# Kernel tuning notes

Measured on AMD Instinct MI355X. Metric: run time of the kernel, lower is better.

The kernel has to match this reference:

```python
import jax, jax.numpy as jnp
import numpy as np

B, H, W = 1, 352, 1216
T = 6          # prop_time
CG = 8         # guidance channels per step
K = 9          # 3x3 propagation kernel


def _conv(x, w, b, pad, groups=1):
    out = jax.lax.conv_general_dilated(
        x, w, (1, 1), [(pad, pad), (pad, pad)],
        dimension_numbers=('NCHW', 'OIHW', 'NCHW'),
        feature_group_count=groups)
    return out if b is None else out + b[None, :, None, None]


def setup_inputs() -> dict:
    key = jax.random.key(0)
    ks = iter(jax.random.split(key, 32))
    def r(shape, s=0.1):
        return jax.random.normal(next(ks), shape, jnp.float32) * s
    return dict(
        feat_init=r((B, 1, H, W), 1.0),
        guidance=r((B, T * CG, H, W), 1.0),
        attn=r((B, 16, H, W), 1.0),
        feat_fix=r((B, 1, H, W), 1.0),
        aff_w_w=r((T, K, CG, 3, 3)), aff_w_b=r((T, K)),
        aff_o_w=r((T, 2 * (K - 1), CG, 3, 3)), aff_o_b=r((T, 2 * (K - 1))),
        proj_w=r((6, 3, 1, 1)),
        bn_gamma=jnp.ones((6,), jnp.float32), bn_beta=jnp.zeros((6,), jnp.float32),
        bn_mean=jnp.zeros((6,), jnp.float32), bn_var=jnp.ones((6,), jnp.float32),
        lsk0_w=r((22, 1, 1, 1)), lsk0_b=r((22,)),
        lsks_w=r((22, 1, 3, 3)), lsks_b=r((22,)),
        lsk1_w=r((11, 22, 1, 1)), lsk1_b=r((11,)),
        lsk2_w=r((11, 22, 1, 1)), lsk2_b=r((11,)),
        lsksq_w=r((2, 2, 3, 3)), lsksq_b=r((2,)),
        lskc_w=r((3, 11, 1, 1)), lskc_b=r((3,)),
    )


def _forward(feat_init, guidance, attn,
             aff_w_w, aff_w_b, aff_o_w, aff_o_b,
             proj_w, bn_gamma, bn_beta, bn_mean, bn_var,
             lsk0_w, lsk0_b, lsks_w, lsks_b, lsk1_w, lsk1_b,
             lsk2_w, lsk2_b, lsksq_w, lsksq_b, lskc_w, lskc_b):
    Bs, _, Hs, Ws = feat_init.shape
    # split guidance into T chunks of CG channels -> (T,B,CG,H,W)
    g = guidance.reshape(Bs, T, CG, Hs, Ws).transpose(1, 0, 2, 3, 4)

    def aff_fn(g_t, ww, wb, ow, ob):
        w = jax.nn.sigmoid(_conv(g_t, ww, wb, 1))              # (B,9,H,W)
        w = w / (w.sum(1, keepdims=True) + 1e-8)
        o = _conv(g_t, ow, ob, 1).reshape(Bs, K - 1, 2, Hs, Ws)
        zero = jnp.zeros((Bs, 1, 2, Hs, Ws), o.dtype)          # reference pixel
        o = jnp.concatenate([o[:, :4], zero, o[:, 4:]], 1).reshape(Bs, 2 * K, Hs, Ws)
        return o, w

    offs, affs = jax.vmap(aff_fn)(g, aff_w_w, aff_w_b, aff_o_w, aff_o_b)

    # modulated deformable conv, weight = ones(1,1,3,3), bias = 0, stride=1, pad=1
    ky = (jnp.repeat(jnp.arange(3), 3) - 1).astype(feat_init.dtype)  # (9,)
    kx = (jnp.tile(jnp.arange(3), 3) - 1).astype(feat_init.dtype)
    yy = jnp.arange(Hs, dtype=feat_init.dtype)
    xx = jnp.arange(Ws, dtype=feat_init.dtype)
    bidx = jnp.arange(Bs)[:, None, None, None]

    def dcn(feat, off, aff):
        img = feat[:, 0]                                       # (B,H,W)
        ys = yy[None, None, :, None] + ky[None, :, None, None] + off[:, 0::2]
        xs = xx[None, None, None, :] + kx[None, :, None, None] + off[:, 1::2]
        y0 = jnp.floor(ys); x0 = jnp.floor(xs)
        wy = ys - y0; wx = xs - x0
        y0i = y0.astype(jnp.int32); x0i = x0.astype(jnp.int32)
        def g4(yi, xi):
            valid = (yi >= 0) & (yi < Hs) & (xi >= 0) & (xi < Ws)
            v = img[bidx, jnp.clip(yi, 0, Hs - 1), jnp.clip(xi, 0, Ws - 1)]
            return v * valid.astype(v.dtype)
        samp = (g4(y0i, x0i) * (1 - wy) * (1 - wx)
                + g4(y0i, x0i + 1) * (1 - wy) * wx
                + g4(y0i + 1, x0i) * wy * (1 - wx)
                + g4(y0i + 1, x0i + 1) * wy * wx)
        return (aff * samp).sum(1)[:, None]                    # (B,1,H,W)

    def step(f, ox):
        o, a = ox
        fn = dcn(f, o, a)
        return fn, fn

    _, feats = jax.lax.scan(step, feat_init.astype(jnp.float32), (offs, affs))

    # combine(list_feat[3:6], attn)
    x3 = jnp.concatenate([feats[3], feats[4], feats[5]], 1)    # (B,3,H,W)
    sf = _conv(x3, proj_w, None, 0)                            # conv 3->6, no bias
    sf = (sf - bn_mean[None, :, None, None]) * jax.lax.rsqrt(bn_var + 1e-5)[None, :, None, None] \
         * bn_gamma[None, :, None, None] + bn_beta[None, :, None, None]
    sf = jnp.where(sf >= 0, sf, 0.2 * sf)                      # LeakyReLU(0.2)
    x22 = jnp.concatenate([attn, sf], 1)                       # (B,22,H,W)

    a1 = _conv(x22, lsk0_w, lsk0_b, 0, 22)                     # depthwise 1x1
    a2 = _conv(a1, lsks_w, lsks_b, 1, 22)                      # depthwise 3x3
    a1 = _conv(a1, lsk1_w, lsk1_b, 0)                          # 22->11
    a2 = _conv(a2, lsk2_w, lsk2_b, 0)                          # 22->11
    cat = jnp.concatenate([a1, a2], 1)
    agg = jnp.concatenate([cat.mean(1, keepdims=True), cat.max(1, keepdims=True)], 1)
    sig = jax.nn.sigmoid(_conv(agg, lsksq_w, lsksq_b, 1))
    at = a1 * sig[:, 0:1] + a2 * sig[:, 1:2]
    at = _conv(at, lskc_w, lskc_b, 0)                          # 11->3
    return (x3 * at).sum(1, keepdims=True)                     # (B,1,H,W)


def reference(feat_init, guidance, attn, feat_fix,
              aff_w_w, aff_w_b, aff_o_w, aff_o_b,
              proj_w, bn_gamma, bn_beta, bn_mean, bn_var,
              lsk0_w, lsk0_b, lsks_w, lsks_b, lsk1_w, lsk1_b,
              lsk2_w, lsk2_b, lsksq_w, lsksq_b, lskc_w, lskc_b):
    # feat_fix only feeds an unused mask path (if False branch) in the original
    return _forward(feat_init, guidance, attn,
                    aff_w_w, aff_w_b, aff_o_w, aff_o_b,
                    proj_w, bn_gamma, bn_beta, bn_mean, bn_var,
                    lsk0_w, lsk0_b, lsks_w, lsks_b, lsk1_w, lsk1_b,
                    lsk2_w, lsk2_b, lsksq_w, lsksq_b, lskc_w, lskc_b)
```

## Files before the change

### kernel.cpp

```cpp
#include <hip/hip_runtime.h>
#include <hip/hip_bf16.h>

#define HH 352
#define WW 1216
#define HWSZ (HH * WW)
#define TT 6

#define WS_CW   16
#define WS_TW   11008
#define WS_FB   12032

typedef __attribute__((ext_vector_type(4))) float f32x4;
typedef __attribute__((ext_vector_type(8))) short s16x8;
union FU { unsigned int u[4]; s16x8 v; };

__device__ inline float ld_in(const void* p, long long i, int bf) {
    return bf ? __bfloat162float(((const __hip_bfloat16*)p)[i]) : ((const float*)p)[i];
}

__device__ inline unsigned int bfsplit_pack(float v) {
    unsigned int uv = __float_as_uint(v);
    unsigned int h = (uv + 0x7FFFu + ((uv >> 16) & 1u)) >> 16;
    float hf = __uint_as_float(h << 16);
    float r = v - hf;
    unsigned int ur = __float_as_uint(r);
    unsigned int l = (ur + 0x7FFFu + ((ur >> 16) & 1u)) >> 16;
    return (h & 0xFFFFu) | (l << 16);
}

__device__ inline int detect_mode(const void* guid) {
    const unsigned int* u = (const unsigned int*)guid;
    int cnt = 0;
    for (int i = 0; i < 128; ++i) {
        unsigned int lo = u[i] & 0xFFFFu;
        int e = (int)((lo >> 7) & 0xFF);
        if (e >= 110 && e <= 140) cnt++;
    }
    return (cnt >= 96) ? 1 : 0;
}

__global__ void prep_small(const void* guid,
                           const void* aww, const void* awb, const void* aow, const void* aob,
                           const void* projw, const void* bng, const void* bnb,
                           const void* bnm, const void* bnv,
                           const void* l0w, const void* l0b, const void* lsw, const void* lsb,
                           const void* l1w, const void* l1b, const void* l2w, const void* l2b,
                           const void* sqw, const void* sqb, const void* lcw, const void* lcb,
                           float* ws) {
    __shared__ int smode;
    if (threadIdx.x == 0) {
        int mode = detect_mode(guid);
        smode = mode;
        if (blockIdx.x == 0) *(int*)ws = mode;
    }
    __syncthreads();
    const int bf = smode;
    const int tid = blockIdx.x * blockDim.x + threadIdx.x;
    const int stp = gridDim.x * blockDim.x;
    float* cw = ws + WS_CW;
    for (int idx = tid; idx < TT * 9 * 72; idx += stp) {
        int t = idx / 648; int r = idx % 648;
        int co = r / 72; int ci = (r % 72) / 9; int tap = r % 9;
        cw[t * 1825 + 25 + co * 72 + ci * 9 + tap] = ld_in(aww, idx, bf);
    }
    for (int idx = tid; idx < TT * 16 * 72; idx += stp) {
        int t = idx / 1152; int r = idx % 1152;
        int co = r / 72; int ci = (r % 72) / 9; int tap = r % 9;
        cw[t * 1825 + 25 + (9 + co) * 72 + ci * 9 + tap] = ld_in(aow, idx, bf);
    }
    for (int idx = tid; idx < TT * 9; idx += stp)
        cw[(idx / 9) * 1825 + (idx % 9)] = ld_in(awb, idx, bf);
    for (int idx = tid; idx < TT * 16; idx += stp)
        cw[(idx / 16) * 1825 + 9 + (idx % 16)] = ld_in(aob, idx, bf);

    float* tw = ws + WS_TW;
    for (int i = tid; i < 18; i += stp) tw[i] = ld_in(projw, i, bf);
    for (int i = tid; i < 6; i += stp) {
        float sc = ld_in(bng, i, bf) * rsqrtf(ld_in(bnv, i, bf) + 1e-5f);
        tw[18 + i] = sc;
        tw[24 + i] = ld_in(bnb, i, bf) - ld_in(bnm, i, bf) * sc;
    }
    for (int i = tid; i < 22;  i += stp) tw[32  + i] = ld_in(l0w, i, bf);
    for (int i = tid; i < 22;  i += stp) tw[54  + i] = ld_in(l0b, i, bf);
    for (int i = tid; i < 198; i += stp) tw[76  + i] = ld_in(lsw, i, bf);
    for (int i = tid; i < 22;  i += stp) tw[274 + i] = ld_in(lsb, i, bf);
    for (int i = tid; i < 242; i += stp) tw[296 + i] = ld_in(l1w, i, bf);
    for (int i = tid; i < 11;  i += stp) tw[538 + i] = ld_in(l1b, i, bf);
    for (int i = tid; i < 242; i += stp) tw[549 + i] = ld_in(l2w, i, bf);
    for (int i = tid; i < 11;  i += stp) tw[791 + i] = ld_in(l2b, i, bf);
    for (int i = tid; i < 36;  i += stp) tw[802 + i] = ld_in(sqw, i, bf);
    for (int i = tid; i < 2;   i += stp) tw[838 + i] = ld_in(sqb, i, bf);
    for (int i = tid; i < 33;  i += stp) tw[840 + i] = ld_in(lcw, i, bf);
    for (int i = tid; i < 3;   i += stp) tw[873 + i] = ld_in(lcb, i, bf);
}

__global__ void prep_feat(const void* __restrict__ feat_init, const int* __restrict__ flagp,
                          float* __restrict__ dst) {
    int bf = *flagp;
    int i = blockIdx.x * 256 + threadIdx.x;
    if (i < HWSZ) dst[i] = ld_in(feat_init, i, bf);
}

__device__ inline float samp(const float* __restrict__ src, int y, int x) {
    bool valid = (y >= 0) & (y < HH) & (x >= 0) & (x < WW);
    int yc = min(max(y, 0), HH - 1);
    int xc = min(max(x, 0), WW - 1);
    float v = src[yc * WW + xc];
    return valid ? v : 0.0f;
}

__global__ __launch_bounds__(256) void dcn_fused(
        const void* __restrict__ guid, const int* __restrict__ flagp,
        const float* __restrict__ wts,
        const float* __restrict__ src, float* __restrict__ dst, int t) {
    __shared__ unsigned int hal[8][10][36];
    __shared__ float outb[4][64][27];
    const int bf = *flagp;
    const int bx = blockIdx.x % 38, by = blockIdx.x / 38;
    const int x0 = bx * 32, y0 = by * 8;
    for (int idx = threadIdx.x; idx < 8 * 360; idx += 256) {
        int ci = idx / 360; int r = (idx % 360) / 36; int c = idx % 36;
        int gy = y0 - 1 + r, gx = x0 - 1 + c;
        float v = 0.f;
        if (c < 34 && gy >= 0 && gy < HH && gx >= 0 && gx < WW)
            v = ld_in(guid, (long long)(t * 8 + ci) * HWSZ + gy * WW + gx, bf);
        hal[ci][r][c] = bfsplit_pack(v);
    }
    const int lane = threadIdx.x & 63;
    const int wave = threadIdx.x >> 6;
    const int col = lane & 15, g = lane >> 4;

    FU Bh[2][3], Bl[2][3];
#pragma unroll
    for (int Nt = 0; Nt < 2; ++Nt)
#pragma unroll
    for (int c = 0; c < 3; ++c) {
        unsigned short eh[8], el[8];
#pragma unroll
        for (int j = 0; j < 8; ++j) {
            int ci = 2 * g + (j >> 2), dx = j & 3;
            int cc = Nt * 16 + col;
            float w = 0.f;
            if (cc < 25 && dx < 3) w = wts[25 + cc * 72 + ci * 9 + c * 3 + dx];
            unsigned int pk = bfsplit_pack(w);
            eh[j] = (unsigned short)(pk & 0xFFFFu);
            el[j] = (unsigned short)(pk >> 16);
        }
#pragma unroll
        for (int q = 0; q < 4; ++q) {
            Bh[Nt][c].u[q] = (unsigned int)eh[2*q] | ((unsigned int)eh[2*q+1] << 16);
            Bl[Nt][c].u[q] = (unsigned int)el[2*q] | ((unsigned int)el[2*q+1] << 16);
        }
    }
    __syncthreads();

    const float* bias = wts;
#pragma unroll
    for (int m = 0; m < 4; ++m) {
        const int M = wave * 4 + m;
        const int py = M >> 1;
        const int pxx = (M & 1) * 16 + col;
        FU Ah[3], Al[3];
#pragma unroll
        for (int c = 0; c < 3; ++c) {
            const unsigned int* r0 = &hal[2 * g][py + c][pxx];
            const unsigned int* r1 = &hal[2 * g + 1][py + c][pxx];
            unsigned int q0 = r0[0], q1 = r0[1], q2 = r0[2], q3 = r0[3];
            unsigned int q4 = r1[0], q5 = r1[1], q6 = r1[2], q7 = r1[3];
            Ah[c].u[0] = __builtin_amdgcn_perm(q1, q0, 0x05040100u);
            Ah[c].u[1] = __builtin_amdgcn_perm(q3, q2, 0x05040100u);
            Ah[c].u[2] = __builtin_amdgcn_perm(q5, q4, 0x05040100u);
            Ah[c].u[3] = __builtin_amdgcn_perm(q7, q6, 0x05040100u);
            Al[c].u[0] = __builtin_amdgcn_perm(q1, q0, 0x07060302u);
            Al[c].u[1] = __builtin_amdgcn_perm(q3, q2, 0x07060302u);
            Al[c].u[2] = __builtin_amdgcn_perm(q5, q4, 0x07060302u);
            Al[c].u[3] = __builtin_amdgcn_perm(q7, q6, 0x07060302u);
        }
#pragma unroll
        for (int Nt = 0; Nt < 2; ++Nt) {
            f32x4 acc = {0.f, 0.f, 0.f, 0.f};
#pragma unroll
            for (int c = 0; c < 3; ++c) {
                acc = __builtin_amdgcn_mfma_f32_16x16x32_bf16(Ah[c].v, Bh[Nt][c].v, acc, 0, 0, 0);
                acc = __builtin_amdgcn_mfma_f32_16x16x32_bf16(Al[c].v, Bh[Nt][c].v, acc, 0, 0, 0);
                acc = __builtin_amdgcn_mfma_f32_16x16x32_bf16(Ah[c].v, Bl[Nt][c].v, acc, 0, 0, 0);
            }
            const int co = Nt * 16 + col;
            if (co < 25) {
                float bs = bias[co];
#pragma unroll
                for (int r = 0; r < 4; ++r)
                    outb[wave][m * 16 + g * 4 + r][co] = acc[r] + bs;
            }
        }
    }
    __syncthreads();
    {
        const int pl = lane;
        const int Ml = pl >> 4, rd = pl & 15;
        const int M = wave * 4 + Ml;
        const int py = M >> 1;
        const int pxx = (M & 1) * 16 + rd;
        const int gy = y0 + py, gx = x0 + pxx;
        float v[25];
#pragma unroll
        for (int c = 0; c < 25; ++c) v[c] = outb[wave][pl][c];
        float w9[9], s = 0.f;
#pragma unroll
        for (int k = 0; k < 9; ++k) { w9[k] = 1.f / (1.f + __expf(-v[k])); s += w9[k]; }
        const float inv = 1.f / (s + 1e-8f);
        float out = 0.f;
#pragma unroll
        for (int k = 0; k < 9; ++k) {
            float oy = 0.f, ox = 0.f;
            if (k != 4) {
                int kp = (k < 4) ? k : (k - 1);
                oy = v[9 + 2 * kp];
                ox = v[10 + 2 * kp];
            }
            float ys = (float)(gy + k / 3 - 1) + oy;
            float xs = (float)(gx + k % 3 - 1) + ox;
            float yf = floorf(ys), xf = floorf(xs);
            float wy = ys - yf, wx = xs - xf;
            int yi = (int)yf, xi = (int)xf;
            float v00 = samp(src, yi, xi);
            float v01 = samp(src, yi, xi + 1);
            float v10 = samp(src, yi + 1, xi);
            float v11 = samp(src, yi + 1, xi + 1);
            float sv = v00 * (1.f - wy) * (1.f - wx) + v01 * (1.f - wy) * wx
                     + v10 * wy * (1.f - wx) + v11 * wy * wx;
            out = fmaf(w9[k] * inv, sv, out);
        }
        dst[gy * WW + gx] = out;
    }
}

__global__ __launch_bounds__(256) void tail1(
        const void* __restrict__ attn, const int* __restrict__ flagp,
        const float* __restrict__ tw, const float* __restrict__ feats,
        float* __restrict__ a1) {
    const int bf = *flagp;
    const int p = blockIdx.x * 256 + threadIdx.x;
    float x3[3] = { feats[3 * HWSZ + p], feats[4 * HWSZ + p], feats[5 * HWSZ + p] };
    float sf[6];
#pragma unroll
    for (int j = 0; j < 6; ++j) {
        float v = tw[j * 3 + 0] * x3[0] + tw[j * 3 + 1] * x3[1] + tw[j * 3 + 2] * x3[2];
        v = v * tw[18 + j] + tw[24 + j];
        sf[j] = (v >= 0.0f) ? v : 0.2f * v;
    }
#pragma unroll
    for (int c = 0; c < 22; ++c) {
        float x = (c < 16) ? ld_in(attn, (long long)c * HWSZ + p, bf) : sf[c - 16];
        a1[c * HWSZ + p] = fmaf(x, tw[32 + c], tw[54 + c]);
    }
}

__global__ __launch_bounds__(256) void tail2(
        const float* __restrict__ tw, const float* __restrict__ a1,
        float* __restrict__ a11, float* __restrict__ a21, float* __restrict__ agg) {
    __shared__ float tile[10][34];
    const int bx = blockIdx.x % 38, by = blockIdx.x / 38;
    const int x0 = bx * 32, y0 = by * 8;
    const int lx = threadIdx.x % 32, ly = threadIdx.x / 32;
    float acc1[11], acc2[11];
#pragma unroll
    for (int j = 0; j < 11; ++j) { acc1[j] = tw[538 + j]; acc2[j] = tw[791 + j]; }
    for (int c = 0; c < 22; ++c) {
        __syncthreads();
        for (int idx = threadIdx.x; idx < 340; idx += 256) {
            int r = idx / 34, cc = idx % 34;
            int gy = y0 - 1 + r, gx = x0 - 1 + cc;
            tile[r][cc] = (gy >= 0 && gy < HH && gx >= 0 && gx < WW)
                          ? a1[c * HWSZ + gy * WW + gx] : 0.0f;
        }
        __syncthreads();
        float a1c = tile[ly + 1][lx + 1];
        float a2c = tw[274 + c];
#pragma unroll
        for (int dy = 0; dy < 3; ++dy)
#pragma unroll
            for (int dx = 0; dx < 3; ++dx)
                a2c = fmaf(tile[ly + dy][lx + dx], tw[76 + c * 9 + dy * 3 + dx], a2c);
#pragma unroll
        for (int j = 0; j < 11; ++j) {
            acc1[j] = fmaf(a1c, tw[296 + j * 22 + c], acc1[j]);
            acc2[j] = fmaf(a2c, tw[549 + j * 22 + c], acc2[j]);
        }
    }
    const int p = (y0 + ly) * WW + x0 + lx;
    float s = 0.0f, mx = -1e30f;
#pragma unroll
    for (int j = 0; j < 11; ++j) {
        a11[j * HWSZ + p] = acc1[j];
        a21[j * HWSZ + p] = acc2[j];
        s += acc1[j] + acc2[j];
        mx = fmaxf(mx, fmaxf(acc1[j], acc2[j]));
    }
    agg[p] = s * (1.0f / 22.0f);
    agg[HWSZ + p] = mx;
}

__global__ __launch_bounds__(256) void tail3(
        const int* __restrict__ flagp, const float* __restrict__ tw,
        const float* __restrict__ feats,
        const float* __restrict__ a11, const float* __restrict__ a21,
        const float* __restrict__ agg, void* __restrict__ out) {
    __shared__ float t0[10][34], t1[10][34];
    const int bx = blockIdx.x % 38, by = blockIdx.x / 38;
    const int x0 = bx * 32, y0 = by * 8;
    for (int idx = threadIdx.x; idx < 340; idx += 256) {
        int r = idx / 34, cc = idx % 34;
        int gy = y0 - 1 + r, gx = x0 - 1 + cc;
        bool ok = (gy >= 0 && gy < HH && gx >= 0 && gx < WW);
        t0[r][cc] = ok ? agg[gy * WW + gx] : 0.0f;
        t1[r][cc] = ok ? agg[HWSZ + gy * WW + gx] : 0.0f;
    }
    __syncthreads();
    const int lx = threadIdx.x % 32, ly = threadIdx.x / 32;
    float s0 = tw[838], s1 = tw[839];
#pragma unroll
    for (int dy = 0; dy < 3; ++dy)
#pragma unroll
        for (int dx = 0; dx < 3; ++dx) {
            float v0 = t0[ly + dy][lx + dx], v1 = t1[ly + dy][lx + dx];
            s0 = fmaf(v0, tw[802 + 0 * 18 + 0 * 9 + dy * 3 + dx], s0);
            s0 = fmaf(v1, tw[802 + 0 * 18 + 1 * 9 + dy * 3 + dx], s0);
            s1 = fmaf(v0, tw[802 + 1 * 18 + 0 * 9 + dy * 3 + dx], s1);
            s1 = fmaf(v1, tw[802 + 1 * 18 + 1 * 9 + dy * 3 + dx], s1);
        }
    float sg0 = 1.0f / (1.0f + __expf(-s0));
    float sg1 = 1.0f / (1.0f + __expf(-s1));
    const int p = (y0 + ly) * WW + x0 + lx;
    float at3[3] = { tw[873], tw[874], tw[875] };
#pragma unroll
    for (int j = 0; j < 11; ++j) {
        float at = a11[j * HWSZ + p] * sg0 + a21[j * HWSZ + p] * sg1;
#pragma unroll
        for (int i = 0; i < 3; ++i) at3[i] = fmaf(at, tw[840 + i * 11 + j], at3[i]);
    }
    float o = feats[3 * HWSZ + p] * at3[0] + feats[4 * HWSZ + p] * at3[1]
            + feats[5 * HWSZ + p] * at3[2];
    int bf = *flagp;
    if (bf) ((__hip_bfloat16*)out)[p] = __float2bfloat16(o);
    else    ((float*)out)[p] = o;
}

extern "C" void kernel_launch(void* const* d_in, const int* in_sizes, int n_in,
                              void* d_out, int out_size, void* d_ws, size_t ws_size,
                              hipStream_t stream) {
    (void)in_sizes; (void)n_in; (void)out_size; (void)ws_size;
    float* WSF = (float*)d_ws;
    const int* flagp = (const int*)d_ws;
    float* cw   = WSF + WS_CW;
    float* tw   = WSF + WS_TW;
    float* FB   = WSF + WS_FB;
    float* A1   = FB + 7 * HWSZ;
    float* A11  = A1 + 22 * HWSZ;
    float* A21  = A11 + 11 * HWSZ;
    float* AGG  = A21 + 11 * HWSZ;

    prep_small<<<32, 256, 0, stream>>>(d_in[1],
        d_in[4], d_in[5], d_in[6], d_in[7],
        d_in[8], d_in[9], d_in[10], d_in[11], d_in[12],
        d_in[13], d_in[14], d_in[15], d_in[16],
        d_in[17], d_in[18], d_in[19], d_in[20],
        d_in[21], d_in[22], d_in[23], d_in[24], WSF);
    prep_feat<<<(HWSZ + 255) / 256, 256, 0, stream>>>(d_in[0], flagp, FB + 6 * HWSZ);

    for (int t = 0; t < 6; ++t) {
        const float* src = (t == 0) ? (FB + 6 * HWSZ) : (FB + (t - 1) * HWSZ);
        dcn_fused<<<44 * 38, 256, 0, stream>>>(d_in[1], flagp, cw + t * 1825, src, FB + t * HWSZ, t);
    }
    tail1<<<HWSZ / 256, 256, 0, stream>>>(d_in[2], flagp, tw, FB, A1);
    tail2<<<44 * 38, 256, 0, stream>>>(tw, A1, A11, A21, AGG);
    tail3<<<44 * 38, 256, 0, stream>>>(flagp, tw, FB, A11, A21, AGG, d_out);
}
```

Before: 484.4 us.

## Merge prep kernels, vectorize guidance halo loads, spread DCN taps across lane groups

The two prep kernels become one launch, so feat_init conversion and weight packing share a single dispatch. In fp32 mode the dcn_fused guidance halo is now loaded with float4 reads instead of scalar loads. The deformable sampling epilogue now runs per 16-pixel M tile right after its MMA, with the 9 taps split across the four 16-lane groups and reduced by shuffles. This shrinks the outb buffer and spreads gather latency over more lanes, at the cost of redundant lanes, extra shuffles and a larger grid for the merged prep kernel.

```diff
diff --git a/kernel.cpp b/kernel.cpp
--- a/kernel.cpp
+++ b/kernel.cpp
@@ -39,14 +39,15 @@
     return (cnt >= 96) ? 1 : 0;
 }
 
-__global__ void prep_small(const void* guid,
-                           const void* aww, const void* awb, const void* aow, const void* aob,
-                           const void* projw, const void* bng, const void* bnb,
-                           const void* bnm, const void* bnv,
-                           const void* l0w, const void* l0b, const void* lsw, const void* lsb,
-                           const void* l1w, const void* l1b, const void* l2w, const void* l2b,
-                           const void* sqw, const void* sqb, const void* lcw, const void* lcb,
-                           float* ws) {
+__global__ __launch_bounds__(256) void prep_all(
+        const void* feat_init, const void* guid,
+        const void* aww, const void* awb, const void* aow, const void* aob,
+        const void* projw, const void* bng, const void* bnb,
+        const void* bnm, const void* bnv,
+        const void* l0w, const void* l0b, const void* lsw, const void* lsb,
+        const void* l1w, const void* l1b, const void* l2w, const void* l2b,
+        const void* sqw, const void* sqb, const void* lcw, const void* lcb,
+        float* ws) {
     __shared__ int smode;
     if (threadIdx.x == 0) {
         int mode = detect_mode(guid);
@@ -55,8 +56,13 @@
     }
     __syncthreads();
     const int bf = smode;
-    const int tid = blockIdx.x * blockDim.x + threadIdx.x;
-    const int stp = gridDim.x * blockDim.x;
+    {
+        int i = blockIdx.x * 256 + threadIdx.x;
+        if (i < HWSZ) ws[WS_FB + 6 * HWSZ + i] = ld_in(feat_init, i, bf);
+    }
+    if (blockIdx.x >= 32) return;
+    const int tid = blockIdx.x * 256 + threadIdx.x;
+    const int stp = 32 * 256;
     float* cw = ws + WS_CW;
     for (int idx = tid; idx < TT * 9 * 72; idx += stp) {
         int t = idx / 648; int r = idx % 648;
@@ -94,13 +100,6 @@
     for (int i = tid; i < 3;   i += stp) tw[873 + i] = ld_in(lcb, i, bf);
 }
 
-__global__ void prep_feat(const void* __restrict__ feat_init, const int* __restrict__ flagp,
-                          float* __restrict__ dst) {
-    int bf = *flagp;
-    int i = blockIdx.x * 256 + threadIdx.x;
-    if (i < HWSZ) dst[i] = ld_in(feat_init, i, bf);
-}
-
 __device__ inline float samp(const float* __restrict__ src, int y, int x) {
     bool valid = (y >= 0) & (y < HH) & (x >= 0) & (x < WW);
     int yc = min(max(y, 0), HH - 1);
@@ -114,17 +113,45 @@
         const float* __restrict__ wts,
         const float* __restrict__ src, float* __restrict__ dst, int t) {
     __shared__ unsigned int hal[8][10][36];
-    __shared__ float outb[4][64][27];
+    __shared__ float outb[4][2][16][27];
     const int bf = *flagp;
     const int bx = blockIdx.x % 38, by = blockIdx.x / 38;
     const int x0 = bx * 32, y0 = by * 8;
-    for (int idx = threadIdx.x; idx < 8 * 360; idx += 256) {
-        int ci = idx / 360; int r = (idx % 360) / 36; int c = idx % 36;
-        int gy = y0 - 1 + r, gx = x0 - 1 + c;
-        float v = 0.f;
-        if (c < 34 && gy >= 0 && gy < HH && gx >= 0 && gx < WW)
-            v = ld_in(guid, (long long)(t * 8 + ci) * HWSZ + gy * WW + gx, bf);
-        hal[ci][r][c] = bfsplit_pack(v);
+
+    if (!bf) {
+        const float* gp = (const float*)guid + (long long)(t * 8) * HWSZ;
+        for (int idx = threadIdx.x; idx < 800; idx += 256) {
+            int ci = idx / 100; int rem = idx % 100; int rr = rem / 10; int k = rem % 10;
+            int gy = y0 - 1 + rr;
+            int gxb = x0 - 4 + 4 * k;
+            float vx = 0.f, vy = 0.f, vz = 0.f, vw = 0.f;
+            if (gy >= 0 && gy < HH) {
+                const float* rowp = gp + (long long)ci * HWSZ + (long long)gy * WW;
+                if (gxb >= 0 && gxb + 3 < WW) {
+                    const float4 v4 = *(const float4*)(rowp + gxb);
+                    vx = v4.x; vy = v4.y; vz = v4.z; vw = v4.w;
+                } else {
+                    if (gxb + 0 >= 0 && gxb + 0 < WW) vx = rowp[gxb + 0];
+                    if (gxb + 1 >= 0 && gxb + 1 < WW) vy = rowp[gxb + 1];
+                    if (gxb + 2 >= 0 && gxb + 2 < WW) vz = rowp[gxb + 2];
+                    if (gxb + 3 >= 0 && gxb + 3 < WW) vw = rowp[gxb + 3];
+                }
+            }
+            int c0 = 4 * k - 3;
+            if (c0 + 0 >= 0 && c0 + 0 < 36) hal[ci][rr][c0 + 0] = bfsplit_pack(vx);
+            if (c0 + 1 >= 0 && c0 + 1 < 36) hal[ci][rr][c0 + 1] = bfsplit_pack(vy);
+            if (c0 + 2 >= 0 && c0 + 2 < 36) hal[ci][rr][c0 + 2] = bfsplit_pack(vz);
+            if (c0 + 3 >= 0 && c0 + 3 < 36) hal[ci][rr][c0 + 3] = bfsplit_pack(vw);
+        }
+    } else {
+        for (int idx = threadIdx.x; idx < 8 * 360; idx += 256) {
+            int ci = idx / 360; int r = (idx % 360) / 36; int c = idx % 36;
+            int gy = y0 - 1 + r, gx = x0 - 1 + c;
+            float v = 0.f;
+            if (c < 34 && gy >= 0 && gy < HH && gx >= 0 && gx < WW)
+                v = ld_in(guid, (long long)(t * 8 + ci) * HWSZ + gy * WW + gx, bf);
+            hal[ci][r][c] = bfsplit_pack(v);
+        }
     }
     const int lane = threadIdx.x & 63;
     const int wave = threadIdx.x >> 6;
@@ -159,7 +186,8 @@
     for (int m = 0; m < 4; ++m) {
         const int M = wave * 4 + m;
         const int py = M >> 1;
-        const int pxx = (M & 1) * 16 + col;
+        const int xoff = (M & 1) * 16;
+        const int pxx = xoff + col;
         FU Ah[3], Al[3];
 #pragma unroll
         for (int c = 0; c < 3; ++c) {
@@ -190,48 +218,60 @@
                 float bs = bias[co];
 #pragma unroll
                 for (int r = 0; r < 4; ++r)
-                    outb[wave][m * 16 + g * 4 + r][co] = acc[r] + bs;
+                    outb[wave][m & 1][g * 4 + r][co] = acc[r] + bs;
             }
         }
-    }
-    __syncthreads();
-    {
-        const int pl = lane;
-        const int Ml = pl >> 4, rd = pl & 15;
-        const int M = wave * 4 + Ml;
-        const int py = M >> 1;
-        const int pxx = (M & 1) * 16 + rd;
-        const int gy = y0 + py, gx = x0 + pxx;
-        float v[25];
-#pragma unroll
-        for (int c = 0; c < 25; ++c) v[c] = outb[wave][pl][c];
-        float w9[9], s = 0.f;
-#pragma unroll
-        for (int k = 0; k < 9; ++k) { w9[k] = 1.f / (1.f + __expf(-v[k])); s += w9[k]; }
-        const float inv = 1.f / (s + 1e-8f);
-        float out = 0.f;
-#pragma unroll
-        for (int k = 0; k < 9; ++k) {
-            float oy = 0.f, ox = 0.f;
-            if (k != 4) {
-                int kp = (k < 4) ? k : (k - 1);
-                oy = v[9 + 2 * kp];
-                ox = v[10 + 2 * kp];
+        {
+            const int px = col;
+            const int gy = y0 + py;
+            const int gx = x0 + xoff + px;
+            const float* ob = &outb[wave][m & 1][px][0];
+            float sg[3], oyv[3], oxv[3];
+            float psum = 0.f;
+#pragma unroll
+            for (int i = 0; i < 3; ++i) {
+                int tap = i * 4 + g;
+                bool valid = tap < 9;
+                int tc = valid ? tap : 8;
+                float wv = ob[tc];
+                float sgv = 1.f / (1.f + __expf(-wv));
+                sg[i] = valid ? sgv : 0.f;
+                psum += sg[i];
+                int kp = (tap < 4) ? tap : tap - 1;
+                kp = min(kp, 7);
+                float oy = ob[9 + 2 * kp];
+                float ox = ob[10 + 2 * kp];
+                bool use_off = valid && (tap != 4);
+                oyv[i] = use_off ? oy : 0.f;
+                oxv[i] = use_off ? ox : 0.f;
             }
-            float ys = (float)(gy + k / 3 - 1) + oy;
-            float xs = (float)(gx + k % 3 - 1) + ox;
-            float yf = floorf(ys), xf = floorf(xs);
-            float wy = ys - yf, wx = xs - xf;
-            int yi = (int)yf, xi = (int)xf;
-            float v00 = samp(src, yi, xi);
-            float v01 = samp(src, yi, xi + 1);
-            float v10 = samp(src, yi + 1, xi);
-            float v11 = samp(src, yi + 1, xi + 1);
-            float sv = v00 * (1.f - wy) * (1.f - wx) + v01 * (1.f - wy) * wx
-                     + v10 * wy * (1.f - wx) + v11 * wy * wx;
-            out = fmaf(w9[k] * inv, sv, out);
-        }
-        dst[gy * WW + gx] = out;
+            psum += __shfl_xor(psum, 16);
+            psum += __shfl_xor(psum, 32);
+            const float inv = 1.f / (psum + 1e-8f);
+            float out = 0.f;
+#pragma unroll
+            for (int i = 0; i < 3; ++i) {
+                int tap = min(i * 4 + g, 8);
+                float w = sg[i] * inv;
+                int d3 = tap / 3;
+                int dy = d3 - 1, dx = tap - 3 * d3 - 1;
+                float ys = (float)(gy + dy) + oyv[i];
+                float xs = (float)(gx + dx) + oxv[i];
+                float yf = floorf(ys), xf = floorf(xs);
+                float wy = ys - yf, wx = xs - xf;
+                int yi = (int)yf, xi = (int)xf;
+                float v00 = samp(src, yi, xi);
+                float v01 = samp(src, yi, xi + 1);
+                float v10 = samp(src, yi + 1, xi);
+                float v11 = samp(src, yi + 1, xi + 1);
+                float sv = v00 * (1.f - wy) * (1.f - wx) + v01 * (1.f - wy) * wx
+                         + v10 * wy * (1.f - wx) + v11 * wy * wx;
+                out = fmaf(w, sv, out);
+            }
+            out += __shfl_xor(out, 16);
+            out += __shfl_xor(out, 32);
+            if (g == 0) dst[gy * WW + gx] = out;
+        }
     }
 }
 
@@ -360,13 +400,12 @@
     float* A21  = A11 + 11 * HWSZ;
     float* AGG  = A21 + 11 * HWSZ;
 
-    prep_small<<<32, 256, 0, stream>>>(d_in[1],
+    prep_all<<<1672, 256, 0, stream>>>(d_in[0], d_in[1],
         d_in[4], d_in[5], d_in[6], d_in[7],
         d_in[8], d_in[9], d_in[10], d_in[11], d_in[12],
         d_in[13], d_in[14], d_in[15], d_in[16],
         d_in[17], d_in[18], d_in[19], d_in[20],
         d_in[21], d_in[22], d_in[23], d_in[24], WSF);
-    prep_feat<<<(HWSZ + 255) / 256, 256, 0, stream>>>(d_in[0], flagp, FB + 6 * HWSZ);
 
     for (int t = 0; t < 6; ++t) {
         const float* src = (t == 0) ? (FB + 6 * HWSZ) : (FB + (t - 1) * HWSZ);
```

Measured after the change: 464.6 us. 1.04x faster.
